# Performance work log

Hardware: AMD Instinct MI355X
Metric: run time of the kernel (lower is better)

## Reference

```python
import jax, jax.numpy as jnp
import numpy as np

MX, MY, MZ = 16, 16, 8  # modes_x, modes_y, modes_z
B, S1, S2, S3, I = 4, 64, 64, 40, 32
HID = 2 * I  # factor * dim


def setup_inputs() -> dict:
    key = jax.random.key(0)
    ks = jax.random.split(key, 14)
    s = 0.05
    d = {}
    d["x"] = jax.random.normal(ks[0], (B, S1, S2, S3, I), jnp.float32)
    # 1x1 Conv1d (in_dim -> in_dim)
    d["w_weight"] = jax.random.normal(ks[1], (I, I), jnp.float32) * s
    d["w_bias"] = jax.random.normal(ks[2], (I,), jnp.float32) * s
    # fourier_weight (positive-mode blocks), stored as (..., 2) real/imag like torch
    d["fw_xy"] = jax.random.normal(ks[3], (I, I, MX, MY, 2), jnp.float32) * s
    d["fw_yz"] = jax.random.normal(ks[4], (I, I, MY, MZ, 2), jnp.float32) * s
    d["fw_xz"] = jax.random.normal(ks[5], (I, I, MX, MZ, 2), jnp.float32) * s
    # fourier_weight2 (negative-mode blocks)
    d["fw2_xy"] = jax.random.normal(ks[6], (I, I, MX, MY, 2), jnp.float32) * s
    d["fw2_yz"] = jax.random.normal(ks[7], (I, I, MY, MZ, 2), jnp.float32) * s
    d["fw2_xz"] = jax.random.normal(ks[8], (I, I, MX, MZ, 2), jnp.float32) * s
    # backcast FeedForward: Linear(I->2I), ReLU, Linear(2I->I)
    d["ff_w0"] = jax.random.normal(ks[9], (HID, I), jnp.float32) * s
    d["ff_b0"] = jax.random.normal(ks[10], (HID,), jnp.float32) * s
    d["ff_w1"] = jax.random.normal(ks[11], (I, HID), jnp.float32) * s
    d["ff_b1"] = jax.random.normal(ks[12], (I,), jnp.float32) * s
    return d


def _cplx(w):
    return w[..., 0] + 1j * w[..., 1]


def _forward_fourier(x, w_weight, w_bias, fw_xy, fw_yz, fw_xz, fw2_xy, fw2_yz, fw2_xz):
    xt = jnp.transpose(x, (0, 4, 1, 2, 3))  # b i x y z
    b_, i_, s1, s2, s3 = xt.shape
    # 1x1 conv branch
    x_w = jnp.einsum('oi,bixyz->boxyz', w_weight, xt) + w_bias[None, :, None, None, None]
    # --- xz branch: rfftn over (x, z), real axis = z ---
    ft = jnp.fft.rfftn(xt, axes=(-3, -1))          # (b,i,s1,s2,s3//2+1)
    Z = s3 // 2 + 1
    out = jnp.zeros(ft.shape, ft.dtype)
    out = out.at[:, :, :MX, :, :MZ].set(
        jnp.einsum('bixyz,ioxz->boxyz', ft[:, :, :MX, :, :MZ], _cplx(fw_xz)))
    out = out.at[:, :, :MX, :, Z - MZ:].set(
        jnp.einsum('bixyz,ioxz->boxyz', ft[:, :, :MX, :, Z - MZ:], _cplx(fw2_xz)))
    xz = jnp.fft.irfftn(out, s=(s1, s3), axes=(-3, -1))
    # --- yz branch: rfftn over (y, z), real axis = z ---
    ft = jnp.fft.rfftn(xt, axes=(-2, -1))          # (b,i,s1,s2,s3//2+1)
    out = jnp.zeros(ft.shape, ft.dtype)
    out = out.at[:, :, :, :MY, :MZ].set(
        jnp.einsum('bixyz,ioyz->boxyz', ft[:, :, :, :MY, :MZ], _cplx(fw_yz)))
    out = out.at[:, :, :, :MY, Z - MZ:].set(
        jnp.einsum('bixyz,ioyz->boxyz', ft[:, :, :, :MY, Z - MZ:], _cplx(fw2_yz)))
    yz = jnp.fft.irfftn(out, s=(s2, s3), axes=(-2, -1))
    # --- xy branch: rfftn over (x, y), real axis = y ---
    ft = jnp.fft.rfftn(xt, axes=(-3, -2))          # (b,i,s1,s2//2+1,s3)
    Y = s2 // 2 + 1
    out = jnp.zeros(ft.shape, ft.dtype)
    out = out.at[:, :, :MX, :MY, :].set(
        jnp.einsum('bixyz,ioxy->boxyz', ft[:, :, :MX, :MY, :], _cplx(fw_xy)))
    out = out.at[:, :, :MX, Y - MY:, :].set(
        jnp.einsum('bixyz,ioxy->boxyz', ft[:, :, :MX, Y - MY:, :], _cplx(fw2_xy)))
    xy = jnp.fft.irfftn(out, s=(s1, s2), axes=(-3, -2))
    total = xy + yz + xz + x_w
    return jnp.transpose(total, (0, 2, 3, 4, 1))  # b s1 s2 s3 i


def reference(x, w_weight, w_bias, fw_xy, fw_yz, fw_xz, fw2_xy, fw2_yz, fw2_xz,
              ff_w0, ff_b0, ff_w1, ff_b1):
    h = _forward_fourier(x, w_weight, w_bias, fw_xy, fw_yz, fw_xz, fw2_xy, fw2_yz, fw2_xz)
    # backcast FeedForward (dropout=0, no layer_norm): Linear -> ReLU -> Linear
    h1 = jax.nn.relu(h @ ff_w0.T + ff_b0)
    b = h1 @ ff_w1.T + ff_b1
    return b
```

## Files before the change

### kernel.cpp

```cpp
#include <hip/hip_runtime.h>
#include <math.h>

#define TWO_PI 6.28318530717958647692f
#define NXD 64
#define NYD 64
#define NZD 40
#define CID 32
#define NJZ 16
#define NJY 32

#define R1SLOT 2621440ll
#define R2SLOT 655360ll
#define R3SLOT 2621440ll

typedef __attribute__((ext_vector_type(8))) short short8;
typedef __attribute__((ext_vector_type(4))) float float4v;

__device__ inline unsigned short f2bf(float f) {
  unsigned u = __builtin_bit_cast(unsigned, f);
  unsigned r = (u + 0x7fffu + ((u >> 16) & 1u)) >> 16;
  return (unsigned short)r;
}
__device__ inline float bf2f(unsigned short h) {
  return __builtin_bit_cast(float, (unsigned)h << 16);
}

__global__ __launch_bounds__(256) void k_conv_mfma(const float* __restrict__ X,
    const float* __restrict__ Wc, const float* __restrict__ bias,
    float* __restrict__ out) {
  int t = threadIdx.x;
  int wid = t >> 6, lane = t & 63;
  int l15 = lane & 15, quad = lane >> 4;
  short8 B[2];
  float bb[2];
  for (int nt = 0; nt < 2; ++nt) {
    int o = nt * 16 + l15;
    for (int j = 0; j < 8; ++j) B[nt][j] = (short)f2bf(Wc[o * 32 + quad * 8 + j]);
    bb[nt] = bias[o];
  }
  const int TOT = 40960;
  int wg = blockIdx.x * 4 + wid;
  for (int tt = wg; tt < TOT; tt += gridDim.x * 4) {
    long r0 = (long)tt * 16;
    const float4v* p = (const float4v*)(X + (r0 + l15) * 32 + quad * 8);
    float4v x0 = p[0], x1 = p[1];
    short8 a;
    for (int j = 0; j < 4; ++j) { a[j] = (short)f2bf(x0[j]); a[4 + j] = (short)f2bf(x1[j]); }
    for (int nt = 0; nt < 2; ++nt) {
      float4v acc = {0.f, 0.f, 0.f, 0.f};
      acc = __builtin_amdgcn_mfma_f32_16x16x32_bf16(a, B[nt], acc, 0, 0, 0);
      for (int r = 0; r < 4; ++r)
        out[(r0 + quad * 4 + r) * 32 + nt * 16 + l15] = acc[r] + bb[nt];
    }
  }
}

__global__ __launch_bounds__(512) void k_zproj(const float* __restrict__ X,
    float2* __restrict__ Tb, int b0) {
  __shared__ float xs[NZD][CID];
  __shared__ float2 tw[NJZ][NZD];
  int t = threadIdx.x;
  int xy = blockIdx.x;
  int b = b0 + blockIdx.z;
  float2* T = Tb + (long)blockIdx.z * R1SLOT;
  const float* src = X + ((long)(b * 4096 + xy)) * NZD * CID;
  for (int k = t; k < NZD * CID; k += 512) xs[k >> 5][k & 31] = src[k];
  for (int k = t; k < NJZ * NZD; k += 512) {
    int j = k / NZD, z = k % NZD;
    int kz = (j < 8) ? j : j + 5;
    int m = (kz * z) % NZD;
    float s_, c_; sincosf(TWO_PI * m / (float)NZD, &s_, &c_);
    tw[j][z] = make_float2(c_, -s_);
  }
  __syncthreads();
  int j = t >> 5, i = t & 31;
  float2 acc = make_float2(0.f, 0.f);
  for (int z = 0; z < NZD; ++z) {
    float v = xs[z][i];
    float2 w = tw[j][z];
    acc.x += v * w.x; acc.y += v * w.y;
  }
  T[((long)xy * NJZ + j) * CID + i] = acc;
}

__global__ __launch_bounds__(256) void k_fwddft(const float2* __restrict__ inb,
    float2* __restrict__ Ub, long CS, long SS, long JS) {
  __shared__ float2 tw[64];
  int t = threadIdx.x;
  if (t < 64) {
    float s_, c_; sincosf(TWO_PI * t / 64.0f, &s_, &c_);
    tw[t] = make_float2(c_, -s_);
  }
  int j = blockIdx.x, sc = blockIdx.y;
  int J = gridDim.x, SD = gridDim.y * 8;
  int s = sc * 8 + (t >> 5), i = t & 31;
  const float2* in = inb + (long)blockIdx.z * R1SLOT + (long)j * JS + (long)s * SS + i;
  float2 acc[16];
#pragma unroll
  for (int m = 0; m < 16; ++m) acc[m] = make_float2(0.f, 0.f);
  __syncthreads();
  for (int c = 0; c < 64; ++c) {
    float2 v = in[(long)c * CS];
#pragma unroll
    for (int m = 0; m < 16; ++m) {
      float2 w = tw[(m * c) & 63];
      acc[m].x += v.x * w.x - v.y * w.y;
      acc[m].y += v.x * w.y + v.y * w.x;
    }
  }
  float2* U = Ub + (long)blockIdx.z * R3SLOT;
#pragma unroll
  for (int m = 0; m < 16; ++m)
    U[((long)(m * J + j) * SD + s) * 32 + i] = acc[m];
}

__global__ __launch_bounds__(256) void k_mix(const float2* __restrict__ Ub,
    float2* __restrict__ Vb, const float* __restrict__ fw, const float* __restrict__ fw2,
    int jsplit, int JW, long OM, long OJ, long OS, int SD) {
  __shared__ float2 Us[64][32];
  __shared__ float2 Wm[32][32];
  int m = blockIdx.x, j = blockIdx.y, t = threadIdx.x;
  int J = gridDim.y;
  const float2* U = Ub + (long)blockIdx.z * R3SLOT + (long)(m * J + j) * SD * 32;
  for (int k = t; k < SD * 32; k += 256) Us[k >> 5][k & 31] = U[k];
  {
    const float* src = (j < jsplit) ? fw : fw2;
    int jl = (j < jsplit) ? j : j - jsplit;
    for (int k = t; k < 1024; k += 256) {
      int i = k >> 5, o = k & 31;
      const float* p = src + (((i * 32 + o) * 16 + m) * JW + jl) * 2;
      Wm[i][o] = make_float2(p[0], p[1]);
    }
  }
  __syncthreads();
  int o = t & 31, sg = t >> 5;
  float2* V = Vb + (long)blockIdx.z * R2SLOT;
  for (int s = sg; s < SD; s += 8) {
    float2 acc = make_float2(0.f, 0.f);
    for (int i2 = 0; i2 < 32; ++i2) {
      float2 u = Us[s][i2], w = Wm[i2][o];
      acc.x += u.x * w.x - u.y * w.y;
      acc.y += u.x * w.y + u.y * w.x;
    }
    V[(long)m * OM + (long)j * OJ + (long)s * OS + o] = acc;
  }
}

__global__ __launch_bounds__(256) void k_invaxis(const float2* __restrict__ Vb,
    float2* __restrict__ Pb) {
  __shared__ float2 Vs[16][CID];
  __shared__ float2 twp[64];
  int s = blockIdx.x, j = blockIdx.y, t = threadIdx.x;
  const float2* V = Vb + (long)blockIdx.z * R2SLOT;
  float2* P = Pb + (long)blockIdx.z * R3SLOT;
  if (t < 64) {
    float s_, c_; sincosf(TWO_PI * t / 64.0f, &s_, &c_);
    twp[t] = make_float2(c_, s_);
  }
  for (int k = t; k < 512; k += 256) {
    int mm = k >> 5, o = k & 31;
    Vs[mm][o] = V[((long)(mm * 64 + s) * NJZ + j) * CID + o];
  }
  __syncthreads();
  int o = t & 31, vg = t >> 5;
  for (int k = 0; k < 8; ++k) {
    int v = vg + 8 * k;
    float2 acc = make_float2(0.f, 0.f);
    for (int mm = 0; mm < 16; ++mm) {
      float2 w = twp[(mm * v) & 63];
      float2 vv = Vs[mm][o];
      acc.x += vv.x * w.x - vv.y * w.y;
      acc.y += vv.x * w.y + vv.y * w.x;
    }
    P[((long)(v * 64 + s) * NJZ + j) * CID + o] = acc;
  }
}

__global__ __launch_bounds__(256) void k_invzadd_mfma(const float2* __restrict__ Pb,
    float* __restrict__ out, long strideV, long strideS, int b0) {
  __shared__ __align__(16) char smem[21120];
  __shared__ float2 tw40[40];
  unsigned short (*PsH)[40] = (unsigned short(*)[40])smem;
  unsigned short (*PsL)[40] = (unsigned short(*)[40])(smem + 10240);
  float (*Cs)[132] = (float(*)[132])smem;
  int t = threadIdx.x;
  int wid = t >> 6, lane = t & 63;
  int l15 = lane & 15, quad = lane >> 4;
  int b = b0 + blockIdx.z;
  int vv = blockIdx.y;
  int s0 = blockIdx.x * 4;
  if (t < 40) {
    float s_, c_; sincosf(TWO_PI * t / 40.0f, &s_, &c_);
    tw40[t] = make_float2(c_, s_);
  }
  __syncthreads();
  short8 AH[3], AL[3];
  for (int zt = 0; zt < 3; ++zt) {
    int z = zt * 16 + l15;
    for (int j = 0; j < 8; ++j) {
      int k = quad * 8 + j;
      int jz = k >> 1, part = k & 1;
      int kz = (jz < 8) ? jz : jz + 5;
      float2 w = tw40[(kz * z) % 40];
      float cj = (kz == 0 || kz == 20) ? 1.0f : 2.0f;
      cj *= (1.0f / 2560.0f);
      float val = part ? -cj * w.y : cj * w.x;
      unsigned short h = f2bf(val);
      AH[zt][j] = (short)h;
      AL[zt][j] = (short)f2bf(val - bf2f(h));
    }
  }
  const float2* src = Pb + (long)blockIdx.z * R3SLOT + ((long)(vv * 64 + s0) * NJZ) * CID;
  for (int kk = t; kk < 16 * 128; kk += 256) {
    int j = kk >> 7, m = kk & 127;
    int sl = m >> 5, o = m & 31;
    float2 v = src[((long)sl * NJZ + j) * CID + o];
    unsigned short hx = f2bf(v.x), hy = f2bf(v.y);
    unsigned short lx = f2bf(v.x - bf2f(hx)), ly = f2bf(v.y - bf2f(hy));
    *(unsigned*)&PsH[m][2 * j] = (unsigned)hx | ((unsigned)hy << 16);
    *(unsigned*)&PsL[m][2 * j] = (unsigned)lx | ((unsigned)ly << 16);
  }
  __syncthreads();
  short8 bh[2], bl[2];
  for (int mt = 0; mt < 2; ++mt) {
    int mc = wid * 32 + mt * 16;
    bh[mt] = *(const short8*)&PsH[mc + l15][quad * 8];
    bl[mt] = *(const short8*)&PsL[mc + l15][quad * 8];
  }
  __syncthreads();
  for (int mt = 0; mt < 2; ++mt) {
    int mc = wid * 32 + mt * 16;
    for (int zt = 0; zt < 3; ++zt) {
      float4v acc = {0.f, 0.f, 0.f, 0.f};
      acc = __builtin_amdgcn_mfma_f32_16x16x32_bf16(AL[zt], bh[mt], acc, 0, 0, 0);
      acc = __builtin_amdgcn_mfma_f32_16x16x32_bf16(AH[zt], bl[mt], acc, 0, 0, 0);
      acc = __builtin_amdgcn_mfma_f32_16x16x32_bf16(AH[zt], bh[mt], acc, 0, 0, 0);
      for (int r = 0; r < 4; ++r) {
        int z = zt * 16 + quad * 4 + r;
        if (z < 40) Cs[z][mc + l15] = acc[r];
      }
    }
  }
  __syncthreads();
  float* obb = out + (long)b * (NXD * NYD * NZD * CID) + (long)vv * strideV
             + (long)s0 * strideS;
  for (int idx = t; idx < 4 * 40 * 8; idx += 256) {
    int sl = idx / 320, rem = idx - sl * 320;
    int z = rem >> 3, o4 = rem & 7;
    float4v* gp = (float4v*)(obb + (long)sl * strideS + z * 32 + o4 * 4);
    float4v g = *gp;
    float4v c = *(const float4v*)&Cs[z][sl * 32 + o4 * 4];
    g.x += c.x; g.y += c.y; g.z += c.z; g.w += c.w;
    *gp = g;
  }
}

__global__ __launch_bounds__(256) void k_fwdy_mfma(const float* __restrict__ X,
    float2* __restrict__ Sb, int b0) {
  __shared__ unsigned short Xs[256][72];
  __shared__ float2 twtab[64];
  int t = threadIdx.x;
  int wid = t >> 6, lane = t & 63;
  int l15 = lane & 15, quad = lane >> 4;
  int b = b0 + blockIdx.z;
  int x = blockIdx.y;
  int m0 = blockIdx.x * 256;
  if (t < 64) {
    float s_, c_; sincosf(TWO_PI * t / 64.0f, &s_, &c_);
    twtab[t] = make_float2(c_, s_);
  }
  __syncthreads();
  short8 Bf[2][4];
  for (int nt = 0; nt < 4; ++nt) {
    int n = nt * 16 + l15;
    int jy = n >> 1, part = n & 1;
    int ky = (jy < 16) ? jy : jy + 1;
    for (int kt = 0; kt < 2; ++kt)
      for (int j = 0; j < 8; ++j) {
        int y = kt * 32 + quad * 8 + j;
        float2 w = twtab[(ky * y) & 63];
        Bf[kt][nt][j] = (short)f2bf(part ? -w.y : w.x);
      }
  }
  const float* src = X + (((long)b * 64 + x) * 64) * 1280 + m0;
  for (int k = t; k < 64 * 256; k += 256) {
    int y = k >> 8, m = k & 255;
    Xs[m][y] = f2bf(src[(long)y * 1280 + m]);
  }
  __syncthreads();
  float2* S = Sb + (long)blockIdx.z * R1SLOT + (long)x * (NJY * NZD * CID);
  for (int mt = 0; mt < 4; ++mt) {
    int mrow = wid * 64 + mt * 16 + l15;
    short8 a0 = *(const short8*)&Xs[mrow][quad * 8];
    short8 a1 = *(const short8*)&Xs[mrow][32 + quad * 8];
    for (int nt = 0; nt < 4; ++nt) {
      float4v acc = {0.f, 0.f, 0.f, 0.f};
      acc = __builtin_amdgcn_mfma_f32_16x16x32_bf16(a0, Bf[0][nt], acc, 0, 0, 0);
      acc = __builtin_amdgcn_mfma_f32_16x16x32_bf16(a1, Bf[1][nt], acc, 0, 0, 0);
      int n = nt * 16 + l15, jy = n >> 1, part = n & 1;
      for (int r = 0; r < 4; ++r) {
        int m = m0 + wid * 64 + mt * 16 + quad * 4 + r;
        int z = m >> 5, i = m & 31;
        ((float*)&S[((long)jy * NZD + z) * CID + i])[part] = acc[r];
      }
    }
  }
}

__global__ __launch_bounds__(256) void k_invx_xy(const float2* __restrict__ V2b,
    float2* __restrict__ P2b) {
  __shared__ float2 Vs[16][CID];
  __shared__ float2 twp[64];
  int jy = blockIdx.x, z = blockIdx.y, t = threadIdx.x;
  const float2* V2 = V2b + (long)blockIdx.z * R2SLOT;
  float2* P2 = P2b + (long)blockIdx.z * R3SLOT;
  if (t < 64) {
    float s_, c_; sincosf(TWO_PI * t / 64.0f, &s_, &c_);
    twp[t] = make_float2(c_, s_);
  }
  for (int k = t; k < 512; k += 256) {
    int kx = k >> 5, o = k & 31;
    Vs[kx][o] = V2[(((long)kx * NJY + jy) * NZD + z) * CID + o];
  }
  __syncthreads();
  int o = t & 31, xg = t >> 5;
  for (int k = 0; k < 8; ++k) {
    int x = xg + 8 * k;
    float2 acc = make_float2(0.f, 0.f);
    for (int kx = 0; kx < 16; ++kx) {
      float2 w = twp[(kx * x) & 63];
      float2 v = Vs[kx][o];
      acc.x += v.x * w.x - v.y * w.y;
      acc.y += v.x * w.y + v.y * w.x;
    }
    P2[(((long)x * NJY + jy) * NZD + z) * CID + o] = acc;
  }
}

__global__ __launch_bounds__(256) void k_invyadd_mfma(const float2* __restrict__ P2b,
    float* __restrict__ out, int b0) {
  __shared__ __align__(16) char smem[18432];
  __shared__ float2 twtab[64];
  unsigned short (*PsH)[72] = (unsigned short(*)[72])smem;
  unsigned short (*PsL)[72] = (unsigned short(*)[72])(smem + 9216);
  float (*Cs)[68] = (float(*)[68])smem;
  int t = threadIdx.x;
  int wid = t >> 6, lane = t & 63;
  int l15 = lane & 15, quad = lane >> 4;
  int b = b0 + blockIdx.z;
  int x = blockIdx.y;
  int m0 = blockIdx.x * 64;
  if (t < 64) {
    float s_, c_; sincosf(TWO_PI * t / 64.0f, &s_, &c_);
    twtab[t] = make_float2(c_, s_);
  }
  __syncthreads();
  short8 AH[2][4], AL[2][4];
  for (int yt = 0; yt < 4; ++yt) {
    int y = yt * 16 + l15;
    for (int kt = 0; kt < 2; ++kt)
      for (int j = 0; j < 8; ++j) {
        int k = kt * 32 + quad * 8 + j;
        int jy = k >> 1, part = k & 1;
        int ky = (jy < 16) ? jy : jy + 1;
        float2 w = twtab[(ky * y) & 63];
        float cj = (ky == 0 || ky == 32) ? 1.0f : 2.0f;
        cj *= (1.0f / 4096.0f);
        float val = part ? -cj * w.y : cj * w.x;
        unsigned short h = f2bf(val);
        AH[kt][yt][j] = (short)h;
        AL[kt][yt][j] = (short)f2bf(val - bf2f(h));
      }
  }
  const float2* src = P2b + (long)blockIdx.z * R3SLOT + (long)x * (NJY * NZD * CID) + m0;
  for (int kk = t; kk < 32 * 64; kk += 256) {
    int jy = kk >> 6, m = kk & 63;
    float2 v = src[(long)jy * (NZD * CID) + m];
    unsigned short hx = f2bf(v.x), hy = f2bf(v.y);
    unsigned short lx = f2bf(v.x - bf2f(hx)), ly = f2bf(v.y - bf2f(hy));
    *(unsigned*)&PsH[m][2 * jy] = (unsigned)hx | ((unsigned)hy << 16);
    *(unsigned*)&PsL[m][2 * jy] = (unsigned)lx | ((unsigned)ly << 16);
  }
  __syncthreads();
  int mc = wid * 16;
  short8 bh0 = *(const short8*)&PsH[mc + l15][quad * 8];
  short8 bh1 = *(const short8*)&PsH[mc + l15][32 + quad * 8];
  short8 bl0 = *(const short8*)&PsL[mc + l15][quad * 8];
  short8 bl1 = *(const short8*)&PsL[mc + l15][32 + quad * 8];
  __syncthreads();
  for (int yt = 0; yt < 4; ++yt) {
    float4v acc = {0.f, 0.f, 0.f, 0.f};
    acc = __builtin_amdgcn_mfma_f32_16x16x32_bf16(AL[0][yt], bh0, acc, 0, 0, 0);
    acc = __builtin_amdgcn_mfma_f32_16x16x32_bf16(AL[1][yt], bh1, acc, 0, 0, 0);
    acc = __builtin_amdgcn_mfma_f32_16x16x32_bf16(AH[0][yt], bl0, acc, 0, 0, 0);
    acc = __builtin_amdgcn_mfma_f32_16x16x32_bf16(AH[1][yt], bl1, acc, 0, 0, 0);
    acc = __builtin_amdgcn_mfma_f32_16x16x32_bf16(AH[0][yt], bh0, acc, 0, 0, 0);
    acc = __builtin_amdgcn_mfma_f32_16x16x32_bf16(AH[1][yt], bh1, acc, 0, 0, 0);
    for (int r = 0; r < 4; ++r) {
      int y = yt * 16 + quad * 4 + r;
      Cs[y][mc + l15] = acc[r];
    }
  }
  __syncthreads();
  float* ob = out + ((long)(b * 64 + x)) * (NYD * NZD * CID) + m0;
  for (int idx = t; idx < 64 * 16; idx += 256) {
    int y = idx >> 4, f = idx & 15;
    float4v* gp = (float4v*)(ob + (long)y * (NZD * CID) + f * 4);
    float4v g = *gp;
    float4v c = *(const float4v*)&Cs[y][f * 4];
    g.x += c.x; g.y += c.y; g.z += c.z; g.w += c.w;
    *gp = g;
  }
}

__global__ __launch_bounds__(256) void k_ff_mfma(float* __restrict__ out,
    const float* __restrict__ W0, const float* __restrict__ b0,
    const float* __restrict__ W1, const float* __restrict__ b1) {
  __shared__ unsigned short h1s[4][16 * 64];
  int t = threadIdx.x;
  int wid = t >> 6, lane = t & 63;
  int l15 = lane & 15, quad = lane >> 4;
  short8 B1[4];
  float bb0[4];
  for (int nt = 0; nt < 4; ++nt) {
    int hh = nt * 16 + l15;
    for (int j = 0; j < 8; ++j) B1[nt][j] = (short)f2bf(W0[hh * 32 + quad * 8 + j]);
    bb0[nt] = b0[hh];
  }
  short8 B2[2][2];
  float bb1[2];
  for (int k0 = 0; k0 < 2; ++k0)
    for (int nt = 0; nt < 2; ++nt) {
      int o = nt * 16 + l15;
      for (int j = 0; j < 8; ++j)
        B2[k0][nt][j] = (short)f2bf(W1[o * 64 + k0 * 32 + quad * 8 + j]);
    }
  for (int nt = 0; nt < 2; ++nt) bb1[nt] = b1[nt * 16 + l15];

  const int TOT = 40960;
  int wg = blockIdx.x * 4 + wid;
  unsigned short* hs = h1s[wid];
  for (int tt = wg; tt < TOT; tt += gridDim.x * 4) {
    long r0 = (long)tt * 16;
    const float4v* p = (const float4v*)(out + (r0 + l15) * 32 + quad * 8);
    float4v x0 = p[0], x1 = p[1];
    short8 a1;
    for (int j = 0; j < 4; ++j) { a1[j] = (short)f2bf(x0[j]); a1[4 + j] = (short)f2bf(x1[j]); }
    for (int nt = 0; nt < 4; ++nt) {
      float4v acc = {0.f, 0.f, 0.f, 0.f};
      acc = __builtin_amdgcn_mfma_f32_16x16x32_bf16(a1, B1[nt], acc, 0, 0, 0);
      for (int r = 0; r < 4; ++r) {
        float v = acc[r] + bb0[nt];
        v = v > 0.f ? v : 0.f;
        hs[(quad * 4 + r) * 64 + nt * 16 + l15] = f2bf(v);
      }
    }
    short8 a2[2];
    for (int k0 = 0; k0 < 2; ++k0)
      a2[k0] = *(const short8*)&hs[l15 * 64 + k0 * 32 + quad * 8];
    for (int nt = 0; nt < 2; ++nt) {
      float4v acc = {0.f, 0.f, 0.f, 0.f};
      acc = __builtin_amdgcn_mfma_f32_16x16x32_bf16(a2[0], B2[0][nt], acc, 0, 0, 0);
      acc = __builtin_amdgcn_mfma_f32_16x16x32_bf16(a2[1], B2[1][nt], acc, 0, 0, 0);
      for (int r = 0; r < 4; ++r)
        out[(r0 + quad * 4 + r) * 32 + nt * 16 + l15] = acc[r] + bb1[nt];
    }
  }
}

extern "C" void kernel_launch(void* const* d_in, const int* in_sizes, int n_in,
                              void* d_out, int out_size, void* d_ws, size_t ws_size,
                              hipStream_t stream) {
  const float* X       = (const float*)d_in[0];
  const float* w_w     = (const float*)d_in[1];
  const float* w_b     = (const float*)d_in[2];
  const float* fw_xy   = (const float*)d_in[3];
  const float* fw_yz   = (const float*)d_in[4];
  const float* fw_xz   = (const float*)d_in[5];
  const float* fw2_xy  = (const float*)d_in[6];
  const float* fw2_yz  = (const float*)d_in[7];
  const float* fw2_xz  = (const float*)d_in[8];
  const float* ff_w0   = (const float*)d_in[9];
  const float* ff_b0   = (const float*)d_in[10];
  const float* ff_w1   = (const float*)d_in[11];
  const float* ff_b1   = (const float*)d_in[12];
  float* out = (float*)d_out;
  char* ws = (char*)d_ws;

  const size_t need_full = (size_t)(R1SLOT + R2SLOT + R3SLOT) * 4 * 8;
  bool full = ws_size >= need_full;

  float2 *r1, *r2, *r3;
  if (full) {
    r1 = (float2*)ws;
    r2 = (float2*)(ws + (size_t)R1SLOT * 4 * 8);
    r3 = (float2*)(ws + (size_t)(R1SLOT + R2SLOT) * 4 * 8);
  } else {
    r1 = (float2*)ws;
    r2 = (float2*)(ws + (size_t)R1SLOT * 8);
    r3 = (float2*)(ws + (size_t)(R1SLOT + R2SLOT) * 8);
  }

  k_conv_mfma<<<dim3(2560), dim3(256), 0, stream>>>(X, w_w, w_b, out);

  int nz = full ? 4 : 1;
  int nb = full ? 1 : 4;
  for (int b = 0; b < nb; ++b) {
    k_zproj<<<dim3(4096, 1, nz), dim3(512), 0, stream>>>(X, r1, b);
    k_fwddft<<<dim3(16, 8, nz), dim3(256), 0, stream>>>(r1, r3, 32768, 512, 32);
    k_mix<<<dim3(16, 16, nz), dim3(256), 0, stream>>>(r3, r2, fw_xz, fw2_xz,
        8, 8, 32768, 32, 512, 64);
    k_invaxis<<<dim3(64, 16, nz), dim3(256), 0, stream>>>(r2, r3);
    k_invzadd_mfma<<<dim3(16, 64, nz), dim3(256), 0, stream>>>(r3, out, 64 * 40 * 32, 40 * 32, b);
    k_fwddft<<<dim3(16, 8, nz), dim3(256), 0, stream>>>(r1, r3, 512, 32768, 32);
    k_mix<<<dim3(16, 16, nz), dim3(256), 0, stream>>>(r3, r2, fw_yz, fw2_yz,
        8, 8, 32768, 32, 512, 64);
    k_invaxis<<<dim3(64, 16, nz), dim3(256), 0, stream>>>(r2, r3);
    k_invzadd_mfma<<<dim3(16, 64, nz), dim3(256), 0, stream>>>(r3, out, 40 * 32, 64 * 40 * 32, b);
    k_fwdy_mfma<<<dim3(5, 64, nz), dim3(256), 0, stream>>>(X, r1, b);
    k_fwddft<<<dim3(32, 5, nz), dim3(256), 0, stream>>>(r1, r3, 40960, 32, 1280);
    k_mix<<<dim3(16, 32, nz), dim3(256), 0, stream>>>(r3, r2, fw_xy, fw2_xy,
        16, 16, 40960, 1280, 32, 40);
    k_invx_xy<<<dim3(32, 40, nz), dim3(256), 0, stream>>>(r2, r3);
    k_invyadd_mfma<<<dim3(20, 64, nz), dim3(256), 0, stream>>>(r3, out, b);
  }

  k_ff_mfma<<<dim3(2560), dim3(256), 0, stream>>>(out, ff_w0, ff_b0, ff_w1, ff_b1);
}
```

Baseline: 799.5 us.

## Precompute DFT twiddle MFMA fragments once and restage y/z DFT kernels

Adds a small prep kernel that computes the bf16 hi/lo twiddle fragments for the inverse-y, inverse-z and forward-y DFT MFMAs into global tables. Each block then loads these instead of running sincos and conversion loops. The shared-memory staging is changed to packed 32-bit words with odd row strides to avoid bank conflicts. The forward-y kernel now uses 128-column tiles and writes through shared memory so the global stores are coalesced. The cost is one extra launch, plus extra global loads per block and extra barriers.

```diff
diff --git a/kernel.cpp b/kernel.cpp
--- a/kernel.cpp
+++ b/kernel.cpp
@@ -23,6 +23,60 @@
 }
 __device__ inline float bf2f(unsigned short h) {
   return __builtin_bit_cast(float, (unsigned)h << 16);
+}
+
+__device__ __align__(16) unsigned short g_invyAH[2][4][64][8];
+__device__ __align__(16) unsigned short g_invyAL[2][4][64][8];
+__device__ __align__(16) unsigned short g_invzAH[3][64][8];
+__device__ __align__(16) unsigned short g_invzAL[3][64][8];
+__device__ __align__(16) unsigned short g_fwdyB[2][4][64][8];
+
+__global__ __launch_bounds__(256) void k_twprep() {
+  int t = threadIdx.x;
+  if (blockIdx.x == 0) {
+    for (int idx = t; idx < 2 * 4 * 64 * 8; idx += 256) {
+      int j = idx & 7, lane = (idx >> 3) & 63, yt = (idx >> 9) & 3, kt = idx >> 11;
+      int l15 = lane & 15, quad = lane >> 4;
+      int y = yt * 16 + l15;
+      int k = kt * 32 + quad * 8 + j;
+      int jy = k >> 1, part = k & 1;
+      int ky = (jy < 16) ? jy : jy + 1;
+      float s_, c_; sincosf(TWO_PI * ((ky * y) & 63) / 64.0f, &s_, &c_);
+      float cj = (ky == 0 || ky == 32) ? 1.0f : 2.0f;
+      cj *= (1.0f / 4096.0f);
+      float val = part ? -cj * s_ : cj * c_;
+      unsigned short h = f2bf(val);
+      g_invyAH[kt][yt][lane][j] = h;
+      g_invyAL[kt][yt][lane][j] = f2bf(val - bf2f(h));
+    }
+  } else if (blockIdx.x == 1) {
+    for (int idx = t; idx < 2 * 4 * 64 * 8; idx += 256) {
+      int j = idx & 7, lane = (idx >> 3) & 63, nt = (idx >> 9) & 3, kt = idx >> 11;
+      int l15 = lane & 15, quad = lane >> 4;
+      int n = nt * 16 + l15;
+      int jy = n >> 1, part = n & 1;
+      int ky = (jy < 16) ? jy : jy + 1;
+      int y = kt * 32 + quad * 8 + j;
+      float s_, c_; sincosf(TWO_PI * ((ky * y) & 63) / 64.0f, &s_, &c_);
+      g_fwdyB[kt][nt][lane][j] = f2bf(part ? -s_ : c_);
+    }
+  } else {
+    for (int idx = t; idx < 3 * 64 * 8; idx += 256) {
+      int j = idx & 7, lane = (idx >> 3) & 63, zt = idx >> 9;
+      int l15 = lane & 15, quad = lane >> 4;
+      int z = zt * 16 + l15;
+      int k = quad * 8 + j;
+      int jz = k >> 1, part = k & 1;
+      int kz = (jz < 8) ? jz : jz + 5;
+      float s_, c_; sincosf(TWO_PI * ((kz * z) % 40) / 40.0f, &s_, &c_);
+      float cj = (kz == 0 || kz == 20) ? 1.0f : 2.0f;
+      cj *= (1.0f / 2560.0f);
+      float val = part ? -cj * s_ : cj * c_;
+      unsigned short h = f2bf(val);
+      g_invzAH[zt][lane][j] = h;
+      g_invzAL[zt][lane][j] = f2bf(val - bf2f(h));
+    }
+  }
 }
 
 __global__ __launch_bounds__(256) void k_conv_mfma(const float* __restrict__ X,
@@ -178,10 +232,9 @@
 
 __global__ __launch_bounds__(256) void k_invzadd_mfma(const float2* __restrict__ Pb,
     float* __restrict__ out, long strideV, long strideS, int b0) {
-  __shared__ __align__(16) char smem[21120];
-  __shared__ float2 tw40[40];
-  unsigned short (*PsH)[40] = (unsigned short(*)[40])smem;
-  unsigned short (*PsL)[40] = (unsigned short(*)[40])(smem + 10240);
+  __shared__ __align__(16) char smem[21504];
+  unsigned (*PsH)[21] = (unsigned(*)[21])smem;
+  unsigned (*PsL)[21] = (unsigned(*)[21])(smem + 10752);
   float (*Cs)[132] = (float(*)[132])smem;
   int t = threadIdx.x;
   int wid = t >> 6, lane = t & 63;
@@ -189,26 +242,10 @@
   int b = b0 + blockIdx.z;
   int vv = blockIdx.y;
   int s0 = blockIdx.x * 4;
-  if (t < 40) {
-    float s_, c_; sincosf(TWO_PI * t / 40.0f, &s_, &c_);
-    tw40[t] = make_float2(c_, s_);
-  }
-  __syncthreads();
   short8 AH[3], AL[3];
   for (int zt = 0; zt < 3; ++zt) {
-    int z = zt * 16 + l15;
-    for (int j = 0; j < 8; ++j) {
-      int k = quad * 8 + j;
-      int jz = k >> 1, part = k & 1;
-      int kz = (jz < 8) ? jz : jz + 5;
-      float2 w = tw40[(kz * z) % 40];
-      float cj = (kz == 0 || kz == 20) ? 1.0f : 2.0f;
-      cj *= (1.0f / 2560.0f);
-      float val = part ? -cj * w.y : cj * w.x;
-      unsigned short h = f2bf(val);
-      AH[zt][j] = (short)h;
-      AL[zt][j] = (short)f2bf(val - bf2f(h));
-    }
+    AH[zt] = *(const short8*)&g_invzAH[zt][lane][0];
+    AL[zt] = *(const short8*)&g_invzAL[zt][lane][0];
   }
   const float2* src = Pb + (long)blockIdx.z * R3SLOT + ((long)(vv * 64 + s0) * NJZ) * CID;
   for (int kk = t; kk < 16 * 128; kk += 256) {
@@ -217,15 +254,19 @@
     float2 v = src[((long)sl * NJZ + j) * CID + o];
     unsigned short hx = f2bf(v.x), hy = f2bf(v.y);
     unsigned short lx = f2bf(v.x - bf2f(hx)), ly = f2bf(v.y - bf2f(hy));
-    *(unsigned*)&PsH[m][2 * j] = (unsigned)hx | ((unsigned)hy << 16);
-    *(unsigned*)&PsL[m][2 * j] = (unsigned)lx | ((unsigned)ly << 16);
+    PsH[m][j] = (unsigned)hx | ((unsigned)hy << 16);
+    PsL[m][j] = (unsigned)lx | ((unsigned)ly << 16);
   }
   __syncthreads();
   short8 bh[2], bl[2];
   for (int mt = 0; mt < 2; ++mt) {
-    int mc = wid * 32 + mt * 16;
-    bh[mt] = *(const short8*)&PsH[mc + l15][quad * 8];
-    bl[mt] = *(const short8*)&PsL[mc + l15][quad * 8];
+    int mc = wid * 32 + mt * 16 + l15;
+    union { unsigned u[4]; short8 s; } th, tl;
+    for (int c = 0; c < 4; ++c) {
+      th.u[c] = PsH[mc][quad * 4 + c];
+      tl.u[c] = PsL[mc][quad * 4 + c];
+    }
+    bh[mt] = th.s; bl[mt] = tl.s;
   }
   __syncthreads();
   for (int mt = 0; mt < 2; ++mt) {
@@ -257,53 +298,52 @@
 
 __global__ __launch_bounds__(256) void k_fwdy_mfma(const float* __restrict__ X,
     float2* __restrict__ Sb, int b0) {
-  __shared__ unsigned short Xs[256][72];
-  __shared__ float2 twtab[64];
+  __shared__ __align__(16) char smem[35328];
+  unsigned (*Xs)[37] = (unsigned(*)[37])smem;
+  float (*Cs)[69] = (float(*)[69])smem;
   int t = threadIdx.x;
   int wid = t >> 6, lane = t & 63;
   int l15 = lane & 15, quad = lane >> 4;
   int b = b0 + blockIdx.z;
   int x = blockIdx.y;
-  int m0 = blockIdx.x * 256;
-  if (t < 64) {
-    float s_, c_; sincosf(TWO_PI * t / 64.0f, &s_, &c_);
-    twtab[t] = make_float2(c_, s_);
-  }
-  __syncthreads();
+  int m0 = blockIdx.x * 128;
   short8 Bf[2][4];
-  for (int nt = 0; nt < 4; ++nt) {
-    int n = nt * 16 + l15;
-    int jy = n >> 1, part = n & 1;
-    int ky = (jy < 16) ? jy : jy + 1;
-    for (int kt = 0; kt < 2; ++kt)
-      for (int j = 0; j < 8; ++j) {
-        int y = kt * 32 + quad * 8 + j;
-        float2 w = twtab[(ky * y) & 63];
-        Bf[kt][nt][j] = (short)f2bf(part ? -w.y : w.x);
-      }
-  }
+  for (int kt = 0; kt < 2; ++kt)
+    for (int nt = 0; nt < 4; ++nt)
+      Bf[kt][nt] = *(const short8*)&g_fwdyB[kt][nt][lane][0];
   const float* src = X + (((long)b * 64 + x) * 64) * 1280 + m0;
-  for (int k = t; k < 64 * 256; k += 256) {
-    int y = k >> 8, m = k & 255;
-    Xs[m][y] = f2bf(src[(long)y * 1280 + m]);
-  }
-  __syncthreads();
-  float2* S = Sb + (long)blockIdx.z * R1SLOT + (long)x * (NJY * NZD * CID);
-  for (int mt = 0; mt < 4; ++mt) {
-    int mrow = wid * 64 + mt * 16 + l15;
-    short8 a0 = *(const short8*)&Xs[mrow][quad * 8];
-    short8 a1 = *(const short8*)&Xs[mrow][32 + quad * 8];
+  for (int k = t; k < 32 * 128; k += 256) {
+    int y2 = k >> 7, m = k & 127;
+    float v0 = src[(long)(2 * y2) * 1280 + m];
+    float v1 = src[(long)(2 * y2 + 1) * 1280 + m];
+    Xs[m][y2] = (unsigned)f2bf(v0) | ((unsigned)f2bf(v1) << 16);
+  }
+  __syncthreads();
+  short8 a[2][2];
+  for (int mt = 0; mt < 2; ++mt) {
+    int mrow = wid * 32 + mt * 16 + l15;
+    for (int kt = 0; kt < 2; ++kt) {
+      union { unsigned u[4]; short8 s; } tmp;
+      for (int c = 0; c < 4; ++c) tmp.u[c] = Xs[mrow][kt * 16 + quad * 4 + c];
+      a[mt][kt] = tmp.s;
+    }
+  }
+  __syncthreads();
+  for (int mt = 0; mt < 2; ++mt) {
     for (int nt = 0; nt < 4; ++nt) {
       float4v acc = {0.f, 0.f, 0.f, 0.f};
-      acc = __builtin_amdgcn_mfma_f32_16x16x32_bf16(a0, Bf[0][nt], acc, 0, 0, 0);
-      acc = __builtin_amdgcn_mfma_f32_16x16x32_bf16(a1, Bf[1][nt], acc, 0, 0, 0);
-      int n = nt * 16 + l15, jy = n >> 1, part = n & 1;
-      for (int r = 0; r < 4; ++r) {
-        int m = m0 + wid * 64 + mt * 16 + quad * 4 + r;
-        int z = m >> 5, i = m & 31;
-        ((float*)&S[((long)jy * NZD + z) * CID + i])[part] = acc[r];
-      }
-    }
+      acc = __builtin_amdgcn_mfma_f32_16x16x32_bf16(a[mt][0], Bf[0][nt], acc, 0, 0, 0);
+      acc = __builtin_amdgcn_mfma_f32_16x16x32_bf16(a[mt][1], Bf[1][nt], acc, 0, 0, 0);
+      int n = nt * 16 + l15;
+      for (int r = 0; r < 4; ++r)
+        Cs[wid * 32 + mt * 16 + quad * 4 + r][n] = acc[r];
+    }
+  }
+  __syncthreads();
+  float2* S = Sb + (long)blockIdx.z * R1SLOT + (long)x * (NJY * NZD * CID) + m0;
+  for (int idx = t; idx < 32 * 128; idx += 256) {
+    int jy = idx >> 7, m = idx & 127;
+    S[(long)jy * 1280 + m] = make_float2(Cs[m][2 * jy], Cs[m][2 * jy + 1]);
   }
 }
 
@@ -339,10 +379,9 @@
 
 __global__ __launch_bounds__(256) void k_invyadd_mfma(const float2* __restrict__ P2b,
     float* __restrict__ out, int b0) {
-  __shared__ __align__(16) char smem[18432];
-  __shared__ float2 twtab[64];
-  unsigned short (*PsH)[72] = (unsigned short(*)[72])smem;
-  unsigned short (*PsL)[72] = (unsigned short(*)[72])(smem + 9216);
+  __shared__ __align__(16) char smem[18944];
+  unsigned (*PsH)[37] = (unsigned(*)[37])smem;
+  unsigned (*PsL)[37] = (unsigned(*)[37])(smem + 9472);
   float (*Cs)[68] = (float(*)[68])smem;
   int t = threadIdx.x;
   int wid = t >> 6, lane = t & 63;
@@ -350,52 +389,42 @@
   int b = b0 + blockIdx.z;
   int x = blockIdx.y;
   int m0 = blockIdx.x * 64;
-  if (t < 64) {
-    float s_, c_; sincosf(TWO_PI * t / 64.0f, &s_, &c_);
-    twtab[t] = make_float2(c_, s_);
-  }
-  __syncthreads();
-  short8 AH[2][4], AL[2][4];
-  for (int yt = 0; yt < 4; ++yt) {
-    int y = yt * 16 + l15;
-    for (int kt = 0; kt < 2; ++kt)
-      for (int j = 0; j < 8; ++j) {
-        int k = kt * 32 + quad * 8 + j;
-        int jy = k >> 1, part = k & 1;
-        int ky = (jy < 16) ? jy : jy + 1;
-        float2 w = twtab[(ky * y) & 63];
-        float cj = (ky == 0 || ky == 32) ? 1.0f : 2.0f;
-        cj *= (1.0f / 4096.0f);
-        float val = part ? -cj * w.y : cj * w.x;
-        unsigned short h = f2bf(val);
-        AH[kt][yt][j] = (short)h;
-        AL[kt][yt][j] = (short)f2bf(val - bf2f(h));
-      }
-  }
   const float2* src = P2b + (long)blockIdx.z * R3SLOT + (long)x * (NJY * NZD * CID) + m0;
   for (int kk = t; kk < 32 * 64; kk += 256) {
     int jy = kk >> 6, m = kk & 63;
     float2 v = src[(long)jy * (NZD * CID) + m];
     unsigned short hx = f2bf(v.x), hy = f2bf(v.y);
     unsigned short lx = f2bf(v.x - bf2f(hx)), ly = f2bf(v.y - bf2f(hy));
-    *(unsigned*)&PsH[m][2 * jy] = (unsigned)hx | ((unsigned)hy << 16);
-    *(unsigned*)&PsL[m][2 * jy] = (unsigned)lx | ((unsigned)ly << 16);
+    PsH[m][jy] = (unsigned)hx | ((unsigned)hy << 16);
+    PsL[m][jy] = (unsigned)lx | ((unsigned)ly << 16);
   }
   __syncthreads();
   int mc = wid * 16;
-  short8 bh0 = *(const short8*)&PsH[mc + l15][quad * 8];
-  short8 bh1 = *(const short8*)&PsH[mc + l15][32 + quad * 8];
-  short8 bl0 = *(const short8*)&PsL[mc + l15][quad * 8];
-  short8 bl1 = *(const short8*)&PsL[mc + l15][32 + quad * 8];
-  __syncthreads();
+  short8 bh0, bh1, bl0, bl1;
+  {
+    union { unsigned u[4]; short8 s; } t0, t1, t2, t3;
+    for (int c = 0; c < 4; ++c) {
+      t0.u[c] = PsH[mc + l15][quad * 4 + c];
+      t1.u[c] = PsH[mc + l15][16 + quad * 4 + c];
+      t2.u[c] = PsL[mc + l15][quad * 4 + c];
+      t3.u[c] = PsL[mc + l15][16 + quad * 4 + c];
+    }
+    bh0 = t0.s; bh1 = t1.s; bl0 = t2.s; bl1 = t3.s;
+  }
+  __syncthreads();
+#pragma unroll 1
   for (int yt = 0; yt < 4; ++yt) {
+    short8 AH0 = *(const short8*)&g_invyAH[0][yt][lane][0];
+    short8 AH1 = *(const short8*)&g_invyAH[1][yt][lane][0];
+    short8 AL0 = *(const short8*)&g_invyAL[0][yt][lane][0];
+    short8 AL1 = *(const short8*)&g_invyAL[1][yt][lane][0];
     float4v acc = {0.f, 0.f, 0.f, 0.f};
-    acc = __builtin_amdgcn_mfma_f32_16x16x32_bf16(AL[0][yt], bh0, acc, 0, 0, 0);
-    acc = __builtin_amdgcn_mfma_f32_16x16x32_bf16(AL[1][yt], bh1, acc, 0, 0, 0);
-    acc = __builtin_amdgcn_mfma_f32_16x16x32_bf16(AH[0][yt], bl0, acc, 0, 0, 0);
-    acc = __builtin_amdgcn_mfma_f32_16x16x32_bf16(AH[1][yt], bl1, acc, 0, 0, 0);
-    acc = __builtin_amdgcn_mfma_f32_16x16x32_bf16(AH[0][yt], bh0, acc, 0, 0, 0);
-    acc = __builtin_amdgcn_mfma_f32_16x16x32_bf16(AH[1][yt], bh1, acc, 0, 0, 0);
+    acc = __builtin_amdgcn_mfma_f32_16x16x32_bf16(AL0, bh0, acc, 0, 0, 0);
+    acc = __builtin_amdgcn_mfma_f32_16x16x32_bf16(AL1, bh1, acc, 0, 0, 0);
+    acc = __builtin_amdgcn_mfma_f32_16x16x32_bf16(AH0, bl0, acc, 0, 0, 0);
+    acc = __builtin_amdgcn_mfma_f32_16x16x32_bf16(AH1, bl1, acc, 0, 0, 0);
+    acc = __builtin_amdgcn_mfma_f32_16x16x32_bf16(AH0, bh0, acc, 0, 0, 0);
+    acc = __builtin_amdgcn_mfma_f32_16x16x32_bf16(AH1, bh1, acc, 0, 0, 0);
     for (int r = 0; r < 4; ++r) {
       int y = yt * 16 + quad * 4 + r;
       Cs[y][mc + l15] = acc[r];
@@ -501,6 +530,7 @@
     r3 = (float2*)(ws + (size_t)(R1SLOT + R2SLOT) * 8);
   }
 
+  k_twprep<<<dim3(3), dim3(256), 0, stream>>>();
   k_conv_mfma<<<dim3(2560), dim3(256), 0, stream>>>(X, w_w, w_b, out);
 
   int nz = full ? 4 : 1;
@@ -517,7 +547,7 @@
         8, 8, 32768, 32, 512, 64);
     k_invaxis<<<dim3(64, 16, nz), dim3(256), 0, stream>>>(r2, r3);
     k_invzadd_mfma<<<dim3(16, 64, nz), dim3(256), 0, stream>>>(r3, out, 40 * 32, 64 * 40 * 32, b);
-    k_fwdy_mfma<<<dim3(5, 64, nz), dim3(256), 0, stream>>>(X, r1, b);
+    k_fwdy_mfma<<<dim3(10, 64, nz), dim3(256), 0, stream>>>(X, r1, b);
     k_fwddft<<<dim3(32, 5, nz), dim3(256), 0, stream>>>(r1, r3, 40960, 32, 1280);
     k_mix<<<dim3(16, 32, nz), dim3(256), 0, stream>>>(r3, r2, fw_xy, fw2_xy,
         16, 16, 40960, 1280, 32, 40);
```

After: 751.6 us. 1.06x faster.
